# Kernel tuning notes

Measured on AMD Instinct MI355X. Metric: run time of the kernel, lower is better.

Reference implementation:

```python
import jax, jax.numpy as jnp
import numpy as np

N_NODES = 50000
N_EDGES = 1200000
N_OD = 10000
D_NODE = 16
D_EDGE = 8
HID = 64
N_LAYERS = 3
K_MIN = 1.0
K_MAX = 50.0


def setup_inputs() -> dict:
    key = jax.random.key(0)
    ks = jax.random.split(key, 24)
    s = 0.05
    inp = {
        "node_features": jax.random.normal(ks[0], (N_NODES, D_NODE), jnp.float32),
        "edge_index": jax.random.randint(ks[1], (2, N_EDGES), 0, N_NODES, jnp.int32),
        "edge_features": jax.random.normal(ks[2], (N_EDGES, D_EDGE), jnp.float32),
        "od_pairs": jax.random.randint(ks[3], (2, N_OD), 0, N_NODES, jnp.int32),
        "traffic_stats": jax.random.normal(ks[4], (4,), jnp.float32),
        # projections
        "Wn": jax.random.normal(ks[5], (D_NODE, HID), jnp.float32) * s,
        "bn": jnp.zeros((HID,), jnp.float32),
        "We": jax.random.normal(ks[6], (D_EDGE, HID), jnp.float32) * s,
        "be": jnp.zeros((HID,), jnp.float32),
        # stacked GNN layer weights: message MLP on [h_src, e], update MLP on [h, agg]
        "Wm": jax.random.normal(ks[7], (N_LAYERS, 2 * HID, HID), jnp.float32) * s,
        "bm": jnp.zeros((N_LAYERS, HID), jnp.float32),
        "Wu": jax.random.normal(ks[8], (N_LAYERS, 2 * HID, HID), jnp.float32) * s,
        "bu": jnp.zeros((N_LAYERS, HID), jnp.float32),
        # per-flow score MLP on [h_src, h_dst]
        "Ws1": jax.random.normal(ks[9], (2 * HID, HID), jnp.float32) * s,
        "bs1": jnp.zeros((HID,), jnp.float32),
        "Ws2": jax.random.normal(ks[10], (HID, 1), jnp.float32) * s,
        "bs2": jnp.zeros((1,), jnp.float32),
        # DynamicKHead: Linear(HID+4,32) -> ReLU -> Linear(32,16) -> ReLU -> Linear(16,1)
        "Wk1": jax.random.normal(ks[11], (HID + 4, 32), jnp.float32) * s,
        "bk1": jnp.zeros((32,), jnp.float32),
        "Wk2": jax.random.normal(ks[12], (32, 16), jnp.float32) * s,
        "bk2": jnp.zeros((16,), jnp.float32),
        "Wk3": jax.random.normal(ks[13], (16, 1), jnp.float32) * s,
        "bk3": jnp.zeros((1,), jnp.float32),
    }
    return inp


def _forward(node_features, edge_features, traffic_stats,
             Wn, bn, We, be, Wm, bm, Wu, bu,
             Ws1, bs1, Ws2, bs2, Wk1, bk1, Wk2, bk2, Wk3, bk3,
             edge_index, od_pairs):
    relu = jax.nn.relu
    h = relu(node_features @ Wn + bn)          # [N, HID]
    e = relu(edge_features @ We + be)          # [E, HID]
    src, dst = edge_index[0], edge_index[1]
    for l in range(N_LAYERS):
        # gather-compute-scatter message passing with edge features
        m = relu(jnp.concatenate([h[src], e], axis=-1) @ Wm[l] + bm[l])  # [E, HID]
        agg = jax.ops.segment_sum(m, dst, num_segments=N_NODES)          # [N, HID]
        h = relu(jnp.concatenate([h, agg], axis=-1) @ Wu[l] + bu[l]) + h  # residual
    # per-flow scores from OD endpoint embeddings
    hp = jnp.concatenate([h[od_pairs[0]], h[od_pairs[1]]], axis=-1)      # [P, 2*HID]
    scores = (relu(hp @ Ws1 + bs1) @ Ws2 + bs2).squeeze(-1)              # [P]
    # dynamic-K head (dropout = identity in eval)
    graph_embed = h.mean(axis=0)                                          # [HID]
    x = jnp.concatenate([graph_embed, traffic_stats], axis=-1)
    raw = (relu(relu(x @ Wk1 + bk1) @ Wk2 + bk2) @ Wk3 + bk3).squeeze(-1)
    k_continuous = K_MIN + jax.nn.sigmoid(raw) * (K_MAX - K_MIN)
    return scores, k_continuous


def reference(node_features, edge_index, edge_features, od_pairs, traffic_stats,
              Wn, bn, We, be, Wm, bm, Wu, bu,
              Ws1, bs1, Ws2, bs2, Wk1, bk1, Wk2, bk2, Wk3, bk3):
    return _forward(node_features, edge_features, traffic_stats,
                    Wn, bn, We, be, Wm, bm, Wu, bu,
                    Ws1, bs1, Ws2, bs2, Wk1, bk1, Wk2, bk2, Wk3, bk3,
                    edge_index, od_pairs)
```

## Files before the change

### kernel.cpp

```cpp
#include <hip/hip_runtime.h>
#include <hip/hip_bf16.h>

#define OFF_WN   0
#define OFF_BN   1024
#define OFF_WE   1088
#define OFF_BE   1600
#define OFF_WM   1664
#define OFF_BM   26240
#define OFF_WU   26432
#define OFF_BU   51008
#define OFF_WS1  51200
#define OFF_BS1  59392
#define OFF_WS2  59456
#define OFF_BS2  59520
#define OFF_WK1  59521
#define OFF_BK1  61697
#define OFF_WK2  61729
#define OFF_BK2  62241
#define OFF_WK3  62257
#define OFF_BK3  62273
#define OFF_TS   62274
#define OFF_GSUM 62278
#define OFF_FLAG 62344
#define OFF_BSUM 62400
#define OFF_BOFF 62900
#define OFF_H    65536

typedef __attribute__((ext_vector_type(8))) short bfrag;
typedef __attribute__((ext_vector_type(4))) float ffrag;

__device__ __forceinline__ float bf2f(unsigned short u) {
    unsigned int i = ((unsigned int)u) << 16;
    float f;
    __builtin_memcpy(&f, &i, sizeof(f));
    return f;
}
__device__ __forceinline__ float bflo(unsigned int u) {
    unsigned int i = u << 16;
    float f; __builtin_memcpy(&f, &i, sizeof(f)); return f;
}
__device__ __forceinline__ float bfhi(unsigned int u) {
    unsigned int i = u & 0xffff0000u;
    float f; __builtin_memcpy(&f, &i, sizeof(f)); return f;
}
__device__ __forceinline__ unsigned int f2bf_rne(float f) {
    unsigned int u; __builtin_memcpy(&u, &f, 4);
    return (u + 0x7fffu + ((u >> 16) & 1u)) >> 16;
}
__device__ __forceinline__ unsigned int pack2bf(float a, float b) {
    return f2bf_rne(a) | (f2bf_rne(b) << 16);
}
__device__ __forceinline__ unsigned int cvt_pk_bf16(float a, float b) {
    unsigned int r;
    asm("v_cvt_pk_bf16_f32 %0, %1, %2" : "=v"(r) : "v"(a), "v"(b));
    return r;
}

__global__ void detect_dtype_kernel(const unsigned short* __restrict__ nf,
                                    int* __restrict__ flag) {
    int t = threadIdx.x;
    float m = 0.f;
    for (int i = t; i < 1024; i += 64) {
        float v = fabsf(bf2f(nf[i]));
        if (!isnan(v)) m = fmaxf(m, v);
        else m = 1e30f;
    }
    for (int o = 32; o > 0; o >>= 1) m = fmaxf(m, __shfl_down(m, o));
    if (t == 0) flag[0] = (m > 1e6f) ? 1 : 0;
}

struct ConvArgs {
    const void* src[19];
    int off[19];
    int n[19];
};

__global__ __launch_bounds__(256) void convert_all_kernel(
        ConvArgs a, float* __restrict__ ws, const int* __restrict__ flagp) {
    int isf32 = *flagp;
    int ai = blockIdx.y;
    int i  = blockIdx.x * blockDim.x + threadIdx.x;
    if (i < a.n[ai]) {
        float v = isf32 ? ((const float*)a.src[ai])[i]
                        : bf2f(((const unsigned short*)a.src[ai])[i]);
        ws[a.off[ai] + i] = v;
    }
}

__global__ __launch_bounds__(256) void wtrans_prep_kernel(
        const float* __restrict__ ws, short* __restrict__ Wb) {
    int idx = blockIdx.x * 256 + threadIdx.x;
    if (idx < 12288) {
        int l = idx >> 12, rem = idx & 4095, n = rem >> 6, k = rem & 63;
        Wb[idx] = (short)f2bf_rne(ws[OFF_WM + l * 8192 + 4096 + k * 64 + n]);
    } else if (idx < 24576) {
        int j = idx - 12288;
        int l = j >> 12, rem = j & 4095, n = rem >> 6, k = rem & 63;
        Wb[idx] = (short)f2bf_rne(ws[OFF_WM + l * 8192 + k * 64 + n]);
    } else if (idx < 49152) {
        int j = idx - 24576;
        int l = j >> 13, rem = j & 8191, n = rem >> 7, k = rem & 127;
        Wb[idx] = (short)f2bf_rne(ws[OFF_WU + l * 8192 + k * 64 + n]);
    } else if (idx < 51200) {
        int j = idx - 49152;
        int n = j >> 5, k = j & 31;
        Wb[idx] = (k < 8) ? (short)f2bf_rne(ws[OFF_WE + k * 64 + n]) : (short)0;
    } else if (idx < 59392) {
        int j = idx - 51200;
        int n = j >> 7, k = j & 127;
        Wb[idx] = (short)f2bf_rne(ws[OFF_WS1 + k * 64 + n]);
    }
}

__global__ __launch_bounds__(256) void node_proj_kernel(
        const void* __restrict__ nf, const float* __restrict__ ws,
        float* __restrict__ h, int N, const int* __restrict__ flagp) {
    int idx = blockIdx.x * blockDim.x + threadIdx.x;
    if (idx >= N * 64) return;
    int isf32 = *flagp;
    int i = idx >> 6, c = idx & 63;
    const float* Wn = ws + OFF_WN;
    float acc = ws[OFF_BN + c];
    float x[16];
    if (isf32) {
        const float* row = (const float*)nf + (size_t)i * 16;
#pragma unroll
        for (int k = 0; k < 16; ++k) x[k] = row[k];
    } else {
        const unsigned short* row = (const unsigned short*)nf + (size_t)i * 16;
#pragma unroll
        for (int k = 0; k < 16; ++k) x[k] = bf2f(row[k]);
    }
#pragma unroll
    for (int k = 0; k < 16; ++k) acc = fmaf(x[k], Wn[k * 64 + c], acc);
    h[idx] = fmaxf(acc, 0.f);
}

__global__ __launch_bounds__(256) void count_kernel(
        const int* __restrict__ dst, int* __restrict__ deg,
        int* __restrict__ rank, int E, int dorank) {
    int e = blockIdx.x * blockDim.x + threadIdx.x;
    if (e < E) {
        int r = atomicAdd(&deg[dst[e]], 1);
        if (dorank) rank[e] = r;
    }
}

__global__ __launch_bounds__(256) void scan_blocks_kernel(
        const int* __restrict__ deg, int* __restrict__ incl,
        int* __restrict__ bsum, int N) {
    int tid = threadIdx.x;
    int gid = blockIdx.x * 256 + tid;
    int v = (gid < N) ? deg[gid] : 0;
    int lane = tid & 63, w = tid >> 6;
    int x = v;
#pragma unroll
    for (int o = 1; o < 64; o <<= 1) {
        int y = __shfl_up(x, o);
        if (lane >= o) x += y;
    }
    __shared__ int wsum[4];
    __shared__ int woff[4];
    if (lane == 63) wsum[w] = x;
    __syncthreads();
    if (tid == 0) {
        int a = 0;
#pragma unroll
        for (int i = 0; i < 4; ++i) { woff[i] = a; a += wsum[i]; }
    }
    __syncthreads();
    x += woff[w];
    if (gid < N) incl[gid] = x;
    if (tid == 255) bsum[blockIdx.x] = x;
}

__global__ __launch_bounds__(256) void scan_bsum_kernel(
        const int* __restrict__ bsum, int* __restrict__ boff, int nb) {
    __shared__ int sh[256];
    int tid = threadIdx.x;
    int carry = 0;
    for (int base = 0; base < nb; base += 256) {
        int v = (base + tid < nb) ? bsum[base + tid] : 0;
        sh[tid] = v;
        __syncthreads();
        for (int o = 1; o < 256; o <<= 1) {
            int t = (tid >= o) ? sh[tid - o] : 0;
            __syncthreads();
            sh[tid] += t;
            __syncthreads();
        }
        if (base + tid < nb) boff[base + tid] = carry + sh[tid] - v;
        __syncthreads();
        carry += sh[255];
        __syncthreads();
    }
}

__global__ __launch_bounds__(256) void scan_finalize_kernel(
        const int* __restrict__ deg, const int* __restrict__ incl,
        const int* __restrict__ boff, int* __restrict__ out,
        int* __restrict__ cursor, int N, int tailval) {
    int gid = blockIdx.x * 256 + threadIdx.x;
    if (gid < N) {
        int ex = boff[blockIdx.x] + incl[gid] - deg[gid];
        out[gid] = ex;
        cursor[gid] = ex;
    }
    if (gid == 0) out[N] = tailval;
}

__global__ __launch_bounds__(256) void fill_kernel(
        const int* __restrict__ src, const int* __restrict__ dst,
        const void* __restrict__ ef, int* __restrict__ cursor,
        const int* __restrict__ rank, const int* __restrict__ off,
        int* __restrict__ eid, int* __restrict__ srcs,
        float* __restrict__ rec, int E, int big,
        const int* __restrict__ flagp) {
    int e = blockIdx.x * blockDim.x + threadIdx.x;
    if (e >= E) return;
    int d = dst[e];
    if (big) {
        int pos = off[d] + rank[e];
        unsigned p01, p23, p45, p67;
        if (*flagp) {
            const float4* p = (const float4*)ef + (size_t)e * 2;
            float4 a = p[0], b = p[1];
            p01 = pack2bf(a.x, a.y); p23 = pack2bf(a.z, a.w);
            p45 = pack2bf(b.x, b.y); p67 = pack2bf(b.z, b.w);
        } else {
            uint4 r = ((const uint4*)ef)[e];
            p01 = r.x; p23 = r.y; p45 = r.z; p67 = r.w;
        }
        float* o = rec + (size_t)pos * 6;
        *(uint2*)o       = make_uint2((unsigned)src[e], (unsigned)d);
        *(uint2*)(o + 2) = make_uint2(p01, p23);
        *(uint2*)(o + 4) = make_uint2(p45, p67);
    } else {
        int pos = atomicAdd(&cursor[d], 1);
        eid[pos] = e;
        srcs[pos] = src[e];
    }
}

__global__ __launch_bounds__(256) void spans_kernel(
        const int* __restrict__ off, int* __restrict__ spans, int N) {
    int i = blockIdx.x * blockDim.x + threadIdx.x;
    if (i >= N) return;
    int k0 = off[i], k1 = off[i + 1];
    spans[i] = (k1 > k0) ? (((k1 - 1) >> 6) - (k0 >> 6) + 1) : 0;
}

__global__ __launch_bounds__(256) void nodeA_mfma_kernel(
        const short* __restrict__ W1T, const float* __restrict__ bm,
        const float* __restrict__ h, float* __restrict__ A, int N) {
    __shared__ short lds_w[64 * 72];
    __shared__ short lds_x[4][64 * 72];
    const int tid = threadIdx.x, wid = tid >> 6, lane = tid & 63;
    const int r = lane & 15, q = lane >> 4;
    const int nb0 = blockIdx.x * 256 + wid * 64;

#pragma unroll
    for (int j = 0; j < 2; ++j) {
        int f8 = (tid * 2 + j) * 8;
        int row = f8 >> 6, k = f8 & 63;
        *(uint4*)&lds_w[row * 72 + k] = ((const uint4*)W1T)[tid * 2 + j];
    }
    short* xt = &lds_x[wid][0];
#pragma unroll 1
    for (int it = 0; it < 16; ++it) {
        int f4 = it * 64 + lane;
        int node = f4 >> 4, c4 = f4 & 15;
        int gn = nb0 + node; if (gn >= N) gn = N - 1;
        float4 v = ((const float4*)h)[(size_t)gn * 16 + c4];
        *(uint2*)&xt[node * 72 + c4 * 4] =
            make_uint2(pack2bf(v.x, v.y), pack2bf(v.z, v.w));
    }
    __syncthreads();

    bfrag bg[4][2];
#pragma unroll
    for (int ni = 0; ni < 4; ++ni)
#pragma unroll
        for (int ki = 0; ki < 2; ++ki)
            bg[ni][ki] = *(const bfrag*)&lds_w[(ni * 16 + r) * 72 + ki * 32 + q * 8];
    float buv[4];
#pragma unroll
    for (int ni = 0; ni < 4; ++ni) buv[ni] = bm[ni * 16 + r];

    ffrag C[4][4];
#pragma unroll
    for (int mi = 0; mi < 4; ++mi) {
        bfrag af[2];
#pragma unroll
        for (int ki = 0; ki < 2; ++ki)
            af[ki] = *(const bfrag*)&xt[(mi * 16 + r) * 72 + ki * 32 + q * 8];
#pragma unroll
        for (int ni = 0; ni < 4; ++ni) {
            ffrag c = {buv[ni], buv[ni], buv[ni], buv[ni]};
            c = __builtin_amdgcn_mfma_f32_16x16x32_bf16(af[0], bg[ni][0], c, 0, 0, 0);
            c = __builtin_amdgcn_mfma_f32_16x16x32_bf16(af[1], bg[ni][1], c, 0, 0, 0);
            C[mi][ni] = c;
        }
    }
#pragma unroll
    for (int mi = 0; mi < 4; ++mi)
#pragma unroll
        for (int rr = 0; rr < 4; ++rr) {
            int gn = nb0 + mi * 16 + q * 4 + rr;
            if (gn < N) {
#pragma unroll
                for (int ni = 0; ni < 4; ++ni)
                    A[(size_t)gn * 64 + ni * 16 + r] = C[mi][ni][rr];
            }
        }
}

__global__ __launch_bounds__(256, 4) void msg_mfma_red(
        const short* __restrict__ WeT, const float* __restrict__ be,
        const short* __restrict__ WbT, const float* __restrict__ rec,
        const float* __restrict__ A, float* __restrict__ pbuf,
        const int* __restrict__ off, const int* __restrict__ pstart, int E) {
    __shared__ short lds_ev[4][64 * 72];
    __shared__ int   lds_src[4][64];
    const int tid = threadIdx.x;
    const int wid = tid >> 6, lane = tid & 63;
    const int w = blockIdx.x * 4 + wid;
    if (w * 64 >= E) return;
    const int slot = w * 64 + lane;
    const int slotc = (slot < E) ? slot : (E - 1);

    const float* rbase = rec + (size_t)slotc * 6;
    uint2 u0 = *(const uint2*)rbase;
    uint2 u1 = *(const uint2*)(rbase + 2);
    uint2 u2 = *(const uint2*)(rbase + 4);
    int s  = (int)u0.x;
    int di = (int)u0.y;
    int pstv = pstart[di];
    int offv = off[di];
    lds_src[wid][lane] = s;

    short* evb = &lds_ev[wid][0];
    short* evrow = evb + lane * 72;
    *(uint4*)(evrow) = make_uint4(u1.x, u1.y, u2.x, u2.y);
    uint4 z4 = make_uint4(0u, 0u, 0u, 0u);
    *(uint4*)(evrow + 8)  = z4;
    *(uint4*)(evrow + 16) = z4;
    *(uint4*)(evrow + 24) = z4;

    const int r = lane & 15, q = lane >> 4;

    bfrag afe[4];
#pragma unroll
    for (int mi = 0; mi < 4; ++mi)
        afe[mi] = *(const bfrag*)(evb + (mi * 16 + r) * 72 + q * 8);

#pragma unroll
    for (int ni = 0; ni < 4; ++ni) {
        bfrag bge = *(const bfrag*)(WeT + (ni * 16 + r) * 32 + q * 8);
        float4 b4 = *(const float4*)(be + ni * 16 + q * 4);
#pragma unroll
        for (int mi = 0; mi < 4; ++mi) {
            ffrag c = {b4.x, b4.y, b4.z, b4.w};
            c = __builtin_amdgcn_mfma_f32_16x16x32_bf16(bge, afe[mi], c, 0, 0, 0);
            unsigned lo = cvt_pk_bf16(fmaxf(c[0], 0.f), fmaxf(c[1], 0.f));
            unsigned hi = cvt_pk_bf16(fmaxf(c[2], 0.f), fmaxf(c[3], 0.f));
            *(uint2*)(evb + (mi * 16 + r) * 72 + ni * 16 + q * 4) =
                make_uint2(lo, hi);
        }
    }

    bfrag af[4][2];
#pragma unroll
    for (int mi = 0; mi < 4; ++mi)
#pragma unroll
        for (int ki = 0; ki < 2; ++ki)
            af[mi][ki] = *(const bfrag*)(evb + (mi * 16 + r) * 72 + ki * 32 + q * 8);

    const float* ap[4][4];
#pragma unroll
    for (int mi = 0; mi < 4; ++mi) {
        int4 sr = *(const int4*)&lds_src[wid][mi * 16 + q * 4];
        ap[mi][0] = A + (size_t)sr.x * 64 + r;
        ap[mi][1] = A + (size_t)sr.y * 64 + r;
        ap[mi][2] = A + (size_t)sr.z * 64 + r;
        ap[mi][3] = A + (size_t)sr.w * 64 + r;
    }

#pragma unroll
    for (int ni = 0; ni < 4; ++ni) {
        bfrag bg0 = *(const bfrag*)(WbT + (ni * 16 + r) * 64 + q * 8);
        bfrag bg1 = *(const bfrag*)(WbT + (ni * 16 + r) * 64 + 32 + q * 8);
        ffrag C[4];
#pragma unroll
        for (int mi = 0; mi < 4; ++mi) {
            C[mi][0] = ap[mi][0][ni * 16];
            C[mi][1] = ap[mi][1][ni * 16];
            C[mi][2] = ap[mi][2][ni * 16];
            C[mi][3] = ap[mi][3][ni * 16];
        }
#pragma unroll
        for (int mi = 0; mi < 4; ++mi) {
            C[mi] = __builtin_amdgcn_mfma_f32_16x16x32_bf16(af[mi][0], bg0, C[mi], 0, 0, 0);
            C[mi] = __builtin_amdgcn_mfma_f32_16x16x32_bf16(af[mi][1], bg1, C[mi], 0, 0, 0);
        }
#pragma unroll
        for (int mi = 0; mi < 4; ++mi) {
            unsigned lo = cvt_pk_bf16(fmaxf(C[mi][0], 0.f), fmaxf(C[mi][1], 0.f));
            unsigned hi = cvt_pk_bf16(fmaxf(C[mi][2], 0.f), fmaxf(C[mi][3], 0.f));
            *(uint2*)(evb + (ni * 16 + r) * 72 + mi * 16 + q * 4) =
                make_uint2(lo, hi);
        }
    }

    int kmax = E - w * 64; if (kmax > 64) kmax = 64;
    if (kmax < 64) {
        for (int k = kmax; k < 64; ++k) evb[lane * 72 + k] = 0;
    }
    int prevd = __shfl_up(di, 1);
    unsigned long long sm = __ballot(lane != 0 && di != prevd);
    int curp = __shfl(pstv, 0) + (w - (__shfl(offv, 0) >> 6));
    float acc = 0.f;
#pragma unroll
    for (int g = 0; g < 8; ++g) {
        uint4 v = *(const uint4*)(evb + lane * 72 + g * 8);
        float f0 = bflo(v.x), f1 = bfhi(v.x), f2 = bflo(v.y), f3 = bfhi(v.y);
        float f4 = bflo(v.z), f5 = bfhi(v.z), f6 = bflo(v.w), f7 = bfhi(v.w);
        unsigned gm = (unsigned)(sm >> (g * 8)) & 0xffu;
        if (gm == 0) {
            acc += (((f0 + f1) + (f2 + f3)) + ((f4 + f5) + (f6 + f7)));
        } else {
            float fv[8] = {f0, f1, f2, f3, f4, f5, f6, f7};
#pragma unroll
            for (int j = 0; j < 8; ++j) {
                if (gm & (1u << j)) {
                    pbuf[(size_t)curp * 64 + lane] = acc;
                    acc = 0.f;
                    curp = __shfl(pstv, g * 8 + j);
                }
                acc += fv[j];
            }
        }
    }
    pbuf[(size_t)curp * 64 + lane] = acc;
}

__global__ __launch_bounds__(256) void fixup_kernel(
        const float* __restrict__ pbuf, const int* __restrict__ off,
        const int* __restrict__ pstart, float* __restrict__ agg, int N) {
    int tid = blockIdx.x * blockDim.x + threadIdx.x;
    int i = tid >> 2, q = tid & 3;
    if (i >= N) return;
    int k0 = off[i], k1 = off[i + 1];
    float acc[16];
#pragma unroll
    for (int c = 0; c < 16; ++c) acc[c] = 0.f;
    if (k1 > k0) {
        int nsp = ((k1 - 1) >> 6) - (k0 >> 6) + 1;
        int p = pstart[i];
        for (int j = 0; j < nsp; ++j) {
            const float4* pr = (const float4*)(pbuf + (size_t)(p + j) * 64 + q * 16);
#pragma unroll
            for (int c = 0; c < 4; ++c) {
                float4 v = pr[c];
                acc[4 * c] += v.x; acc[4 * c + 1] += v.y;
                acc[4 * c + 2] += v.z; acc[4 * c + 3] += v.w;
            }
        }
    }
    float4* o4 = (float4*)(agg + (size_t)i * 64 + q * 16);
#pragma unroll
    for (int c = 0; c < 4; ++c)
        o4[c] = make_float4(acc[4 * c], acc[4 * c + 1], acc[4 * c + 2], acc[4 * c + 3]);
}

__global__ __launch_bounds__(128) void update_mfma_kernel(
        const short* __restrict__ WuT, const float* __restrict__ bu,
        float* __restrict__ h, const float* __restrict__ agg, int N) {
    __shared__ short lds_w[64 * 136];
    __shared__ short lds_x[2][64 * 136];
    const int tid = threadIdx.x, wid = tid >> 6, lane = tid & 63;
    const int r = lane & 15, q = lane >> 4;
    const int nb0 = blockIdx.x * 128 + wid * 64;
#pragma unroll
    for (int j = 0; j < 8; ++j) {
        int f8 = (tid * 8 + j) * 8;
        int row = f8 >> 7, k = f8 & 127;
        *(uint4*)&lds_w[row * 136 + k] = ((const uint4*)WuT)[tid * 8 + j];
    }
    short* xt = &lds_x[wid][0];
#pragma unroll 1
    for (int it = 0; it < 32; ++it) {
        int f4 = it * 64 + lane;
        int node = f4 >> 5, c4 = f4 & 31;
        int gn = nb0 + node; if (gn >= N) gn = N - 1;
        const float4* src = (c4 < 16)
            ? ((const float4*)h + (size_t)gn * 16 + c4)
            : ((const float4*)agg + (size_t)gn * 16 + (c4 - 16));
        float4 v = *src;
        *(uint2*)&xt[node * 136 + c4 * 4] =
            make_uint2(pack2bf(v.x, v.y), pack2bf(v.z, v.w));
    }
    __syncthreads();
    bfrag bg[4][4];
#pragma unroll
    for (int ni = 0; ni < 4; ++ni)
#pragma unroll
        for (int ki = 0; ki < 4; ++ki)
            bg[ni][ki] = *(const bfrag*)&lds_w[(ni * 16 + r) * 136 + ki * 32 + q * 8];
    float buv[4];
#pragma unroll
    for (int ni = 0; ni < 4; ++ni) buv[ni] = bu[ni * 16 + r];
    ffrag C[4][4];
#pragma unroll
    for (int mi = 0; mi < 4; ++mi) {
        bfrag af[4];
#pragma unroll
        for (int ki = 0; ki < 4; ++ki)
            af[ki] = *(const bfrag*)&xt[(mi * 16 + r) * 136 + ki * 32 + q * 8];
#pragma unroll
        for (int ni = 0; ni < 4; ++ni) {
            ffrag c = {buv[ni], buv[ni], buv[ni], buv[ni]};
#pragma unroll
            for (int ki = 0; ki < 4; ++ki)
                c = __builtin_amdgcn_mfma_f32_16x16x32_bf16(af[ki], bg[ni][ki], c, 0, 0, 0);
            C[mi][ni] = c;
        }
    }
#pragma unroll
    for (int mi = 0; mi < 4; ++mi)
#pragma unroll
        for (int rr = 0; rr < 4; ++rr) {
            int nl = mi * 16 + q * 4 + rr;
            int gn = nb0 + nl;
            if (gn < N) {
#pragma unroll
                for (int ni = 0; ni < 4; ++ni) {
                    float hold = bf2f((unsigned short)xt[nl * 136 + ni * 16 + r]);
                    h[(size_t)gn * 64 + ni * 16 + r] =
                        fmaxf(C[mi][ni][rr], 0.f) + hold;
                }
            }
        }
}

__global__ __launch_bounds__(256) void gather_msg_fallback(
        const float* __restrict__ Wm2, const float* __restrict__ We,
        const float* __restrict__ be, const void* __restrict__ ef,
        const int* __restrict__ srcs, const int* __restrict__ eid,
        const int* __restrict__ off, const float* __restrict__ A,
        float* __restrict__ agg, int N, const int* __restrict__ flagp) {
    int i = blockIdx.x * blockDim.x + threadIdx.x;
    if (i >= N) return;
    int isf32 = *flagp;
    int k0 = off[i], k1 = off[i + 1];
    float acc[64];
#pragma unroll
    for (int c = 0; c < 64; ++c) acc[c] = 0.f;
    for (int k = k0; k < k1; ++k) {
        int s = srcs[k];
        int e = eid[k];
        const float4* a4 = (const float4*)(A + (size_t)s * 64);
        float t[64];
#pragma unroll
        for (int c = 0; c < 16; ++c) {
            float4 v = a4[c];
            t[4 * c] = v.x; t[4 * c + 1] = v.y; t[4 * c + 2] = v.z; t[4 * c + 3] = v.w;
        }
        float efv[8];
        if (isf32) {
            const float4* e4 = (const float4*)ef + (size_t)e * 2;
            float4 ra = e4[0], rb = e4[1];
            efv[0]=ra.x; efv[1]=ra.y; efv[2]=ra.z; efv[3]=ra.w;
            efv[4]=rb.x; efv[5]=rb.y; efv[6]=rb.z; efv[7]=rb.w;
        } else {
            uint4 rr = ((const uint4*)ef)[e];
            efv[0]=bflo(rr.x); efv[1]=bfhi(rr.x); efv[2]=bflo(rr.y); efv[3]=bfhi(rr.y);
            efv[4]=bflo(rr.z); efv[5]=bfhi(rr.z); efv[6]=bflo(rr.w); efv[7]=bfhi(rr.w);
        }
#pragma unroll 1
        for (int d0 = 0; d0 < 64; d0 += 8) {
            float ev[8];
#pragma unroll
            for (int dd = 0; dd < 8; ++dd) {
                float a = be[d0 + dd];
#pragma unroll
                for (int kk = 0; kk < 8; ++kk) a = fmaf(efv[kk], We[kk * 64 + d0 + dd], a);
                ev[dd] = fmaxf(a, 0.f);
            }
#pragma unroll
            for (int dd = 0; dd < 8; ++dd) {
                const float* w = Wm2 + (d0 + dd) * 64;
#pragma unroll
                for (int c = 0; c < 64; ++c) t[c] = fmaf(ev[dd], w[c], t[c]);
            }
        }
#pragma unroll
        for (int c = 0; c < 64; ++c) acc[c] += fmaxf(t[c], 0.f);
    }
    float4* o4 = (float4*)(agg + (size_t)i * 64);
#pragma unroll
    for (int c = 0; c < 16; ++c)
        o4[c] = make_float4(acc[4 * c], acc[4 * c + 1], acc[4 * c + 2], acc[4 * c + 3]);
}

__global__ __launch_bounds__(128) void scores_mfma_kernel(
        const short* __restrict__ Ws1T, const float* __restrict__ bs1,
        const float* __restrict__ Ws2, const float* __restrict__ bs2,
        const int* __restrict__ ods, const int* __restrict__ odd,
        const float* __restrict__ h, void* __restrict__ out, int P,
        const int* __restrict__ flagp) {
    __shared__ short lds_w[64 * 136];
    __shared__ short lds_x[2][64 * 136];
    const int tid = threadIdx.x, wid = tid >> 6, lane = tid & 63;
    const int r = lane & 15, q = lane >> 4;
    const int pb0 = blockIdx.x * 128 + wid * 64;
#pragma unroll
    for (int j = 0; j < 8; ++j) {
        int f8 = (tid * 8 + j) * 8;
        int row = f8 >> 7, k = f8 & 127;
        *(uint4*)&lds_w[row * 136 + k] = ((const uint4*)Ws1T)[tid * 8 + j];
    }
    short* xt = &lds_x[wid][0];
#pragma unroll 1
    for (int it = 0; it < 32; ++it) {
        int f4 = it * 64 + lane;
        int pr = f4 >> 5, c4 = f4 & 31;
        int gp = pb0 + pr; if (gp >= P) gp = P - 1;
        int node = (c4 < 16) ? ods[gp] : odd[gp];
        int cc = (c4 < 16) ? c4 : (c4 - 16);
        float4 v = ((const float4*)h)[(size_t)node * 16 + cc];
        *(uint2*)&xt[pr * 136 + c4 * 4] =
            make_uint2(pack2bf(v.x, v.y), pack2bf(v.z, v.w));
    }
    __syncthreads();

    bfrag bg[4][4];
#pragma unroll
    for (int ni = 0; ni < 4; ++ni)
#pragma unroll
        for (int ki = 0; ki < 4; ++ki)
            bg[ni][ki] = *(const bfrag*)&lds_w[(ni * 16 + r) * 136 + ki * 32 + q * 8];
    float buv[4], w2v[4];
#pragma unroll
    for (int ni = 0; ni < 4; ++ni) { buv[ni] = bs1[ni * 16 + r]; w2v[ni] = Ws2[ni * 16 + r]; }
    int isf32 = *flagp;
    float b2 = bs2[0];

#pragma unroll
    for (int mi = 0; mi < 4; ++mi) {
        bfrag af[4];
#pragma unroll
        for (int ki = 0; ki < 4; ++ki)
            af[ki] = *(const bfrag*)&xt[(mi * 16 + r) * 136 + ki * 32 + q * 8];
        float part[4] = {0.f, 0.f, 0.f, 0.f};
#pragma unroll
        for (int ni = 0; ni < 4; ++ni) {
            ffrag c = {buv[ni], buv[ni], buv[ni], buv[ni]};
#pragma unroll
            for (int ki = 0; ki < 4; ++ki)
                c = __builtin_amdgcn_mfma_f32_16x16x32_bf16(af[ki], bg[ni][ki], c, 0, 0, 0);
#pragma unroll
            for (int rr = 0; rr < 4; ++rr)
                part[rr] = fmaf(fmaxf(c[rr], 0.f), w2v[ni], part[rr]);
        }
#pragma unroll
        for (int rr = 0; rr < 4; ++rr) {
            float v = part[rr];
            v += __shfl_xor(v, 1); v += __shfl_xor(v, 2);
            v += __shfl_xor(v, 4); v += __shfl_xor(v, 8);
            if (r == 0) {
                int p = pb0 + mi * 16 + q * 4 + rr;
                if (p < P) {
                    float score = v + b2;
                    if (isf32) ((float*)out)[p] = score;
                    else ((__hip_bfloat16*)out)[p] = __float2bfloat16(score);
                }
            }
        }
    }
}

__global__ __launch_bounds__(256) void embed_kernel(
        const float* __restrict__ h, float* __restrict__ gsum, int N) {
    __shared__ float red[256];
    int c = threadIdx.x & 63;
    int sub = threadIdx.x >> 6;
    float a = 0.f;
    for (int i = blockIdx.x * 4 + sub; i < N; i += gridDim.x * 4)
        a += h[(size_t)i * 64 + c];
    red[threadIdx.x] = a;
    __syncthreads();
    if (threadIdx.x < 64) {
        float t = red[threadIdx.x] + red[threadIdx.x + 64] +
                  red[threadIdx.x + 128] + red[threadIdx.x + 192];
        unsafeAtomicAdd(&gsum[threadIdx.x], t);
    }
}

__global__ void khead_kernel(const float* __restrict__ ws,
                             void* __restrict__ out, int N, int P,
                             const int* __restrict__ flagp) {
    __shared__ float sh1[32];
    __shared__ float sh2[16];
    int lane = threadIdx.x;
    float invN = 1.f / (float)N;
    float a1 = (lane < 32) ? ws[OFF_BK1 + lane] : 0.f;
#pragma unroll
    for (int i = 0; i < 68; ++i) {
        float xi = (i < 64) ? ws[OFF_GSUM + i] * invN : ws[OFF_TS + i - 64];
        if (lane < 32) a1 = fmaf(xi, ws[OFF_WK1 + i * 32 + lane], a1);
    }
    if (lane < 32) sh1[lane] = fmaxf(a1, 0.f);
    __syncthreads();
    float a2 = (lane < 16) ? ws[OFF_BK2 + lane] : 0.f;
#pragma unroll
    for (int j = 0; j < 32; ++j) {
        if (lane < 16) a2 = fmaf(sh1[j], ws[OFF_WK2 + j * 16 + lane], a2);
    }
    if (lane < 16) sh2[lane] = fmaxf(a2, 0.f);
    __syncthreads();
    if (lane == 0) {
        float raw = ws[OFF_BK3];
#pragma unroll
        for (int k2 = 0; k2 < 16; ++k2) raw = fmaf(sh2[k2], ws[OFF_WK3 + k2], raw);
        float sig = 1.f / (1.f + expf(-raw));
        float k = 1.f + 49.f * sig;
        if (*flagp) ((float*)out)[P] = k;
        else ((__hip_bfloat16*)out)[P] = __float2bfloat16(k);
    }
}

extern "C" void kernel_launch(void* const* d_in, const int* in_sizes, int n_in,
                              void* d_out, int out_size, void* d_ws, size_t ws_size,
                              hipStream_t stream) {
    const void* nf = d_in[0];
    const int*  ei = (const int*)d_in[1];
    const void* ef = d_in[2];
    const int*  od = (const int*)d_in[3];
    float* ws = (float*)d_ws;

    const int N = in_sizes[0] / 16;
    const int E = in_sizes[1] / 2;
    const int P = in_sizes[3] / 2;

    float* h      = ws + OFF_H;
    float* agg    = h + (size_t)N * 64;
    float* A      = agg + (size_t)N * 64;
    int*   deg    = (int*)(A + (size_t)N * 64);
    int*   off    = deg + N;
    int*   cursor = off + N + 1;
    int*   pstart = cursor + N;
    int*   eid    = pstart + N + 1;
    int*   srcs   = eid + E;
    short* WbT    = (short*)(srcs + E);
    short* W1T    = WbT + 12288;
    short* WuT    = WbT + 24576;
    short* WeT    = WbT + 49152;
    short* Ws1T   = WbT + 51200;
    int*   rank   = (int*)(WbT + 59392);
    int*   flag   = (int*)(ws + OFF_FLAG);
    int*   bsum   = (int*)(ws + OFF_BSUM);
    int*   boff   = (int*)(ws + OFF_BOFF);

    size_t fsofar = (size_t)OFF_H + 3 * (size_t)N * 64
                  + (size_t)(N + (N + 1) + N + (N + 1) + E + E + E) + 29696;
    size_t recOff = (fsofar + 7) & ~(size_t)7;
    float* rec = ws + recOff;
    size_t pbufOff = recOff + (size_t)E * 6;
    float* pbuf = ws + pbufOff;
    long pbufRows = (long)N + E / 64 + 128;
    size_t needBytes = (pbufOff + (size_t)pbufRows * 64) * sizeof(float);
    const bool big = (ws_size >= needBytes);

    const int* srcv = ei;
    const int* dstv = ei + E;

    detect_dtype_kernel<<<1, 64, 0, stream>>>((const unsigned short*)nf, flag);

    ConvArgs ca;
    const int srcidx[19] = {5, 6, 7, 8, 9, 10, 11, 12, 13, 14, 15, 16, 17, 18, 19, 20, 21, 22, 4};
    const int wsoff[19]  = {OFF_WN, OFF_BN, OFF_WE, OFF_BE, OFF_WM, OFF_BM, OFF_WU, OFF_BU,
                            OFF_WS1, OFF_BS1, OFF_WS2, OFF_BS2, OFF_WK1, OFF_BK1, OFF_WK2,
                            OFF_BK2, OFF_WK3, OFF_BK3, OFF_TS};
    int maxn = 0;
    for (int i = 0; i < 19; ++i) {
        ca.src[i] = d_in[srcidx[i]];
        ca.off[i] = wsoff[i];
        ca.n[i]   = in_sizes[srcidx[i]];
        if (ca.n[i] > maxn) maxn = ca.n[i];
    }
    dim3 cgrid((maxn + 255) / 256, 19);
    convert_all_kernel<<<cgrid, 256, 0, stream>>>(ca, ws, flag);
    wtrans_prep_kernel<<<232, 256, 0, stream>>>(ws, WbT);

    node_proj_kernel<<<(N * 64 + 255) / 256, 256, 0, stream>>>(nf, ws, h, N, flag);

    hipMemsetAsync(deg, 0, (size_t)N * sizeof(int), stream);
    count_kernel<<<(E + 255) / 256, 256, 0, stream>>>(dstv, deg, rank, E, big ? 1 : 0);
    int nb = (N + 255) / 256;
    scan_blocks_kernel<<<nb, 256, 0, stream>>>(deg, cursor, bsum, N);
    scan_bsum_kernel<<<1, 256, 0, stream>>>(bsum, boff, nb);
    scan_finalize_kernel<<<nb, 256, 0, stream>>>(deg, cursor, boff, off, cursor, N, E);
    fill_kernel<<<(E + 255) / 256, 256, 0, stream>>>(
        srcv, dstv, ef, cursor, rank, off, eid, srcs, rec, E, big ? 1 : 0, flag);

    if (big) {
        spans_kernel<<<nb, 256, 0, stream>>>(off, deg, N);
        scan_blocks_kernel<<<nb, 256, 0, stream>>>(deg, cursor, bsum, N);
        scan_bsum_kernel<<<1, 256, 0, stream>>>(bsum, boff, nb);
        scan_finalize_kernel<<<nb, 256, 0, stream>>>(deg, cursor, boff, pstart, cursor, N, 0);
    }

    const int N4 = N * 4;
    const int mblocks = (E + 255) / 256;
    const int ablocks = (N + 255) / 256;
    const int ublocks = (N + 127) / 128;
    for (int l = 0; l < 3; ++l) {
        nodeA_mfma_kernel<<<ablocks, 256, 0, stream>>>(
            W1T + l * 4096, ws + OFF_BM + l * 64, h, A, N);
        if (big) {
            msg_mfma_red<<<mblocks, 256, 0, stream>>>(
                WeT, ws + OFF_BE, WbT + l * 4096, rec, A, pbuf, off, pstart, E);
            fixup_kernel<<<(N4 + 255) / 256, 256, 0, stream>>>(
                pbuf, off, pstart, agg, N);
        } else {
            const float* Wm2 = ws + OFF_WM + l * 8192 + 4096;
            gather_msg_fallback<<<(N + 255) / 256, 256, 0, stream>>>(
                Wm2, ws + OFF_WE, ws + OFF_BE, ef, srcs, eid, off, A, agg, N, flag);
        }
        update_mfma_kernel<<<ublocks, 128, 0, stream>>>(
            WuT + l * 8192, ws + OFF_BU + l * 64, h, agg, N);
    }

    scores_mfma_kernel<<<(P + 127) / 128, 128, 0, stream>>>(
        Ws1T, ws + OFF_BS1, ws + OFF_WS2, ws + OFF_BS2,
        od, od + P, h, d_out, P, flag);

    hipMemsetAsync(ws + OFF_GSUM, 0, 64 * sizeof(float), stream);
    embed_kernel<<<256, 256, 0, stream>>>(h, ws + OFF_GSUM, N);
    khead_kernel<<<1, 64, 0, stream>>>(ws, d_out, N, P, flag);
}
```

Before: 562.6 us.

## Replace atomic-rank CSR fill with two-pass bucketed scatter

The CSR build drops the per-edge global rank from count_kernel. Edges are now scattered in two passes: first into coarse 256-node buckets using an LDS histogram and one global atomic per bucket per block, then within each bucket using LDS atomics into the final record slots. The aim is better locality for the 24-byte record writes and fewer global atomics. In exchange it adds a round trip through an intermediate buffer (aliased on pbuf), an extra launch and a memset, and bcur holds only 256 entries, which limits N to 65536 nodes.

Result: slower. 582.9 us (+3.6%).

```diff
diff --git a/kernel.cpp b/kernel.cpp
--- a/kernel.cpp
+++ b/kernel.cpp
@@ -24,6 +24,7 @@
 #define OFF_FLAG 62344
 #define OFF_BSUM 62400
 #define OFF_BOFF 62900
+#define OFF_BCUR 63300
 #define OFF_H    65536
 
 typedef __attribute__((ext_vector_type(8))) short bfrag;
@@ -137,13 +138,9 @@
 }
 
 __global__ __launch_bounds__(256) void count_kernel(
-        const int* __restrict__ dst, int* __restrict__ deg,
-        int* __restrict__ rank, int E, int dorank) {
+        const int* __restrict__ dst, int* __restrict__ deg, int E) {
     int e = blockIdx.x * blockDim.x + threadIdx.x;
-    if (e < E) {
-        int r = atomicAdd(&deg[dst[e]], 1);
-        if (dorank) rank[e] = r;
-    }
+    if (e < E) atomicAdd(&deg[dst[e]], 1);
 }
 
 __global__ __launch_bounds__(256) void scan_blocks_kernel(
@@ -209,20 +206,42 @@
     if (gid == 0) out[N] = tailval;
 }
 
-__global__ __launch_bounds__(256) void fill_kernel(
+
+__global__ __launch_bounds__(256) void fill_passA(
         const int* __restrict__ src, const int* __restrict__ dst,
-        const void* __restrict__ ef, int* __restrict__ cursor,
-        const int* __restrict__ rank, const int* __restrict__ off,
-        int* __restrict__ eid, int* __restrict__ srcs,
-        float* __restrict__ rec, int E, int big,
+        const void* __restrict__ ef, const int* __restrict__ off,
+        int* __restrict__ bcur, float* __restrict__ interm, int E, int N,
         const int* __restrict__ flagp) {
-    int e = blockIdx.x * blockDim.x + threadIdx.x;
-    if (e >= E) return;
-    int d = dst[e];
-    if (big) {
-        int pos = off[d] + rank[e];
+    __shared__ int hist[256];
+    __shared__ int gbase[256];
+    const int tid = threadIdx.x;
+    const int base = blockIdx.x * 4096;
+    const int nbk = (N + 255) >> 8;
+    hist[tid] = 0;
+    __syncthreads();
+    int dd[16], lr[16];
+#pragma unroll
+    for (int j = 0; j < 16; ++j) {
+        int e = base + j * 256 + tid;
+        if (e < E) {
+            int d = dst[e];
+            dd[j] = d;
+            lr[j] = atomicAdd(&hist[d >> 8], 1);
+        } else dd[j] = -1;
+    }
+    __syncthreads();
+    if (tid < nbk && hist[tid] > 0) {
+        int g = atomicAdd(&bcur[tid], hist[tid]);
+        gbase[tid] = off[tid << 8] + g;
+    }
+    __syncthreads();
+    int isf32 = *flagp;
+#pragma unroll
+    for (int j = 0; j < 16; ++j) {
+        int e = base + j * 256 + tid;
+        if (e >= E) continue;
         unsigned p01, p23, p45, p67;
-        if (*flagp) {
+        if (isf32) {
             const float4* p = (const float4*)ef + (size_t)e * 2;
             float4 a = p[0], b = p[1];
             p01 = pack2bf(a.x, a.y); p23 = pack2bf(a.z, a.w);
@@ -231,15 +250,49 @@
             uint4 r = ((const uint4*)ef)[e];
             p01 = r.x; p23 = r.y; p45 = r.z; p67 = r.w;
         }
-        float* o = rec + (size_t)pos * 6;
-        *(uint2*)o       = make_uint2((unsigned)src[e], (unsigned)d);
+        int pos = gbase[dd[j] >> 8] + lr[j];
+        float* o = interm + (size_t)pos * 6;
+        *(uint2*)o       = make_uint2((unsigned)src[e], (unsigned)dd[j]);
         *(uint2*)(o + 2) = make_uint2(p01, p23);
         *(uint2*)(o + 4) = make_uint2(p45, p67);
-    } else {
-        int pos = atomicAdd(&cursor[d], 1);
-        eid[pos] = e;
-        srcs[pos] = src[e];
-    }
+    }
+}
+
+__global__ __launch_bounds__(256) void fill_passB(
+        const float* __restrict__ interm, const int* __restrict__ off,
+        float* __restrict__ rec, int N) {
+    __shared__ int cur[256];
+    const int b = blockIdx.x;
+    const int beg = b << 8;
+    const int end = (beg + 256 < N) ? beg + 256 : N;
+    const int span = end - beg;
+    const int tid = threadIdx.x;
+    if (tid < span) cur[tid] = off[beg + tid];
+    __syncthreads();
+    const int k0 = off[beg];
+    const int k1 = off[end];
+    for (int i = k0 + tid; i < k1; i += 256) {
+        const float* ip = interm + (size_t)i * 6;
+        uint2 a  = *(const uint2*)ip;
+        uint2 bq = *(const uint2*)(ip + 2);
+        uint2 c  = *(const uint2*)(ip + 4);
+        int slot = atomicAdd(&cur[(int)a.y - beg], 1);
+        float* o = rec + (size_t)slot * 6;
+        *(uint2*)o       = a;
+        *(uint2*)(o + 2) = bq;
+        *(uint2*)(o + 4) = c;
+    }
+}
+
+__global__ __launch_bounds__(256) void fill_fallback(
+        const int* __restrict__ src, const int* __restrict__ dst,
+        int* __restrict__ cursor, int* __restrict__ eid,
+        int* __restrict__ srcs, int E) {
+    int e = blockIdx.x * blockDim.x + threadIdx.x;
+    if (e >= E) return;
+    int pos = atomicAdd(&cursor[dst[e]], 1);
+    eid[pos] = e;
+    srcs[pos] = src[e];
 }
 
 __global__ __launch_bounds__(256) void spans_kernel(
@@ -757,19 +810,23 @@
     short* WuT    = WbT + 24576;
     short* WeT    = WbT + 49152;
     short* Ws1T   = WbT + 51200;
-    int*   rank   = (int*)(WbT + 59392);
     int*   flag   = (int*)(ws + OFF_FLAG);
     int*   bsum   = (int*)(ws + OFF_BSUM);
     int*   boff   = (int*)(ws + OFF_BOFF);
+    int*   bcur   = (int*)(ws + OFF_BCUR);
 
     size_t fsofar = (size_t)OFF_H + 3 * (size_t)N * 64
-                  + (size_t)(N + (N + 1) + N + (N + 1) + E + E + E) + 29696;
+                  + (size_t)(N + (N + 1) + N + (N + 1) + E + E) + 29696;
     size_t recOff = (fsofar + 7) & ~(size_t)7;
     float* rec = ws + recOff;
     size_t pbufOff = recOff + (size_t)E * 6;
     float* pbuf = ws + pbufOff;
+    float* interm = pbuf;
     long pbufRows = (long)N + E / 64 + 128;
-    size_t needBytes = (pbufOff + (size_t)pbufRows * 64) * sizeof(float);
+    size_t tailFloats = (size_t)pbufRows * 64;
+    size_t intermFloats = (size_t)E * 6;
+    if (intermFloats > tailFloats) tailFloats = intermFloats;
+    size_t needBytes = (pbufOff + tailFloats) * sizeof(float);
     const bool big = (ws_size >= needBytes);
 
     const int* srcv = ei;
@@ -796,13 +853,20 @@
     node_proj_kernel<<<(N * 64 + 255) / 256, 256, 0, stream>>>(nf, ws, h, N, flag);
 
     hipMemsetAsync(deg, 0, (size_t)N * sizeof(int), stream);
-    count_kernel<<<(E + 255) / 256, 256, 0, stream>>>(dstv, deg, rank, E, big ? 1 : 0);
+    count_kernel<<<(E + 255) / 256, 256, 0, stream>>>(dstv, deg, E);
     int nb = (N + 255) / 256;
     scan_blocks_kernel<<<nb, 256, 0, stream>>>(deg, cursor, bsum, N);
     scan_bsum_kernel<<<1, 256, 0, stream>>>(bsum, boff, nb);
     scan_finalize_kernel<<<nb, 256, 0, stream>>>(deg, cursor, boff, off, cursor, N, E);
-    fill_kernel<<<(E + 255) / 256, 256, 0, stream>>>(
-        srcv, dstv, ef, cursor, rank, off, eid, srcs, rec, E, big ? 1 : 0, flag);
+    if (big) {
+        hipMemsetAsync(bcur, 0, 256 * sizeof(int), stream);
+        fill_passA<<<(E + 4095) / 4096, 256, 0, stream>>>(
+            srcv, dstv, ef, off, bcur, interm, E, N, flag);
+        fill_passB<<<(N + 255) / 256, 256, 0, stream>>>(interm, off, rec, N);
+    } else {
+        fill_fallback<<<(E + 255) / 256, 256, 0, stream>>>(
+            srcv, dstv, cursor, eid, srcs, E);
+    }
 
     if (big) {
         spans_kernel<<<nb, 256, 0, stream>>>(off, deg, N);
```
